# Optimization experiments

Measured on AMD Instinct MI355X. Metric: run time of the kernel, lower is better.

## Reference

```python
import jax, jax.numpy as jnp
import numpy as np

B, N, C, CP, H, NK = 1, 2048, 128, 16, 8, 128
D = C // H
W_HALF = NK // 2
EPS = 1e-5
NEG = -1e9


def _ln(x, scale=None, bias=None):
    m = jnp.mean(x, axis=-1, keepdims=True)
    v = jnp.var(x, axis=-1, keepdims=True)
    y = (x - m) * jax.lax.rsqrt(v + EPS)
    if scale is not None:
        y = y * scale
    if bias is not None:
        y = y + bias
    return y


def _ada_ln(a, s, s_scale, gate_w, gate_b, skip_w):
    # AF3 AdaLN: a <- sigmoid(Lin(LN(s))) * LN(a) + LinNoBias(LN(s))
    sn = _ln(s, s_scale)
    return jax.nn.sigmoid(sn @ gate_w + gate_b) * _ln(a) + sn @ skip_w


def setup_inputs() -> dict:
    key = jax.random.key(0)
    ks = jax.random.split(key, 24)

    def w(k, shape, fan_in):
        return jax.random.normal(k, shape, jnp.float32) / np.float32(np.sqrt(fan_in))

    return {
        'atom_single_repr': jax.random.normal(ks[0], (B, N, C), jnp.float32),
        'atom_single_proj': jax.random.normal(ks[1], (B, N, C), jnp.float32),
        'atom_pair_repr': jax.random.normal(ks[2], (B, N, N, CP), jnp.float32),
        'mask': jnp.ones((B, N), jnp.float32),
        # AttentionPairBias AdaLN
        'adaln_s_scale': jnp.ones((C,), jnp.float32),
        'adaln_gate_w': w(ks[3], (C, C), C),
        'adaln_gate_b': jnp.zeros((C,), jnp.float32),
        'adaln_skip_w': w(ks[4], (C, C), C),
        # attention projections
        'wq': w(ks[5], (C, H * D), C),
        'wk': w(ks[6], (C, H * D), C),
        'wv': w(ks[7], (C, H * D), C),
        'wg': w(ks[8], (C, H * D), C),
        'bg': jnp.ones((H * D,), jnp.float32),
        'wo': w(ks[9], (H * D, C), H * D),
        'bo': jnp.zeros((C,), jnp.float32),
        # pair bias
        'pair_ln_scale': jnp.ones((CP,), jnp.float32),
        'pair_ln_bias': jnp.zeros((CP,), jnp.float32),
        'w_pair': w(ks[10], (CP, H), CP),
        # adaLN-zero output gate (bias init -2)
        'out_gate_w': w(ks[11], (C, C), C),
        'out_gate_b': jnp.full((C,), -2.0, jnp.float32),
        # ConditionedTransitionBlock AdaLN
        't_s_scale': jnp.ones((C,), jnp.float32),
        't_gate_w': w(ks[12], (C, C), C),
        't_gate_b': jnp.zeros((C,), jnp.float32),
        't_skip_w': w(ks[13], (C, C), C),
        # SwiGLU transition, expansion n=2
        't_swish_w': w(ks[14], (C, 2 * C), C),
        't_hidden_w': w(ks[15], (C, 2 * C), C),
        't_out_w': w(ks[16], (2 * C, C), 2 * C),
        't_out_gate_w': w(ks[17], (C, C), C),
        't_out_gate_b': jnp.full((C,), -2.0, jnp.float32),
    }


def reference(atom_single_repr, atom_single_proj, atom_pair_repr, mask,
              adaln_s_scale, adaln_gate_w, adaln_gate_b, adaln_skip_w,
              wq, wk, wv, wg, bg, wo, bo,
              pair_ln_scale, pair_ln_bias, w_pair,
              out_gate_w, out_gate_b,
              t_s_scale, t_gate_w, t_gate_b, t_skip_w,
              t_swish_w, t_hidden_w, t_out_w, t_out_gate_w, t_out_gate_b):
    b, n, _ = atom_single_repr.shape
    # --- AttentionPairBias ---
    a = _ada_ln(atom_single_repr, atom_single_proj,
                adaln_s_scale, adaln_gate_w, adaln_gate_b, adaln_skip_w)
    # pair bias [b,h,n,n]
    bias = jnp.transpose(_ln(atom_pair_repr, pair_ln_scale, pair_ln_bias) @ w_pair, (0, 3, 1, 2))
    idx = jnp.arange(n)
    diff = idx[None, :] - idx[:, None]  # j - i
    win = (diff >= -W_HALF) & (diff <= W_HALF)  # sliding window (left,right)=(64,64)
    bias = bias + jnp.where(win, 0.0, NEG)[None, None]
    bias = bias + (1e9 * (mask - 1.0))[:, None, None, :]
    q = (a @ wq).reshape(b, n, H, D) * (D ** -0.5)
    k = (a @ wk).reshape(b, n, H, D)
    v = (a @ wv).reshape(b, n, H, D)
    attn = jax.nn.softmax(jnp.einsum('bqhd,bkhd->bhqk', q, k) + bias, axis=-1)
    o = jnp.einsum('bhqk,bkhd->bqhd', attn, v)
    g = jax.nn.sigmoid(a @ wg + bg).reshape(b, n, H, D)  # per-head output gating
    attn_out = (o * g).reshape(b, n, H * D) @ wo + bo
    attn_out = jax.nn.sigmoid(atom_single_proj @ out_gate_w + out_gate_b) * attn_out
    # --- ConditionedTransitionBlock ---
    t = _ada_ln(atom_single_repr, atom_single_proj,
                t_s_scale, t_gate_w, t_gate_b, t_skip_w)
    hid = jax.nn.silu(t @ t_swish_w) * (t @ t_hidden_w)  # SwiGLU
    trans = jax.nn.sigmoid(atom_single_proj @ t_out_gate_w + t_out_gate_b) * (hid @ t_out_w)
    return attn_out + trans
```

## Files before the change

kernel.cpp:

```cpp
#include <hip/hip_runtime.h>

#define NN 2048
#define CC 128
#define CPC 16
#define HH 8
#define DD 16
#define WHALF 64

__device__ __forceinline__ float sigf(float x){ return 1.0f/(1.0f+__expf(-x)); }

__global__ __launch_bounds__(256) void ln_both(const float* __restrict__ a,
                                               const float* __restrict__ s,
                                               float* __restrict__ ln_a,
                                               float* __restrict__ ln_s){
  const float* x = blockIdx.y ? s : a;
  float* ln = blockIdx.y ? ln_s : ln_a;
  int row = blockIdx.x*4 + (threadIdx.x>>6);
  int lane = threadIdx.x & 63;
  size_t base = (size_t)row*CC;
  float2 v = *(const float2*)(x + base + 2*lane);
  float ssum = v.x+v.y, sq = v.x*v.x+v.y*v.y;
  #pragma unroll
  for (int m=32;m;m>>=1){ ssum += __shfl_xor(ssum,m); sq += __shfl_xor(sq,m); }
  float mean = ssum*(1.0f/CC);
  float var  = sq*(1.0f/CC)-mean*mean;
  float inv  = rsqrtf(var+1e-5f);
  float2 o; o.x=(v.x-mean)*inv; o.y=(v.y-mean)*inv;
  *(float2*)(ln + base + 2*lane) = o;
}

template<int K, int RPT, int NM>
__device__ __forceinline__ void gemm_core(const float* __restrict__ Arows,
                                          const float* __restrict__ scale,
                                          const float* __restrict__ W0,
                                          const float* __restrict__ W1,
                                          int ldw, int colBase,
                                          float acc[NM][RPT][4], float* As){
  const int t = threadIdx.x;
  constexpr int ROWS = RPT*8;
  const int nv = ROWS*K/4;
  for (int i=t;i<nv;i+=256){
    float4 v = ((const float4*)Arows)[i];
    if (scale){
      int kk = (i*4)&(K-1);
      v.x*=scale[kk]; v.y*=scale[kk+1]; v.z*=scale[kk+2]; v.w*=scale[kk+3];
    }
    ((float4*)As)[i]=v;
  }
  __syncthreads();
  const int tr = t>>5;
  const int col = colBase + (t&31)*4;
  #pragma unroll
  for(int m=0;m<NM;m++)
    #pragma unroll
    for(int r=0;r<RPT;r++){ acc[m][r][0]=0;acc[m][r][1]=0;acc[m][r][2]=0;acc[m][r][3]=0; }
  #pragma unroll 4
  for (int k=0;k<K;k++){
    float a[RPT];
    #pragma unroll
    for (int r=0;r<RPT;r++) a[r]=As[(tr*RPT+r)*K+k];
    {
      float4 w = *(const float4*)(W0 + (size_t)k*ldw + col);
      #pragma unroll
      for (int r=0;r<RPT;r++){acc[0][r][0]+=a[r]*w.x;acc[0][r][1]+=a[r]*w.y;acc[0][r][2]+=a[r]*w.z;acc[0][r][3]+=a[r]*w.w;}
    }
    if constexpr (NM>1){
      float4 w = *(const float4*)(W1 + (size_t)k*ldw + col);
      #pragma unroll
      for (int r=0;r<RPT;r++){acc[1][r][0]+=a[r]*w.x;acc[1][r][1]+=a[r]*w.y;acc[1][r][2]+=a[r]*w.z;acc[1][r][3]+=a[r]*w.w;}
    }
  }
}

__global__ __launch_bounds__(256) void k_gates(const float* __restrict__ s,
    const float* __restrict__ W0, const float* __restrict__ b0,
    const float* __restrict__ W1, const float* __restrict__ b1,
    float* __restrict__ sgog, float* __restrict__ sgtg){
  __shared__ float As[8*128];
  float acc[2][1][4];
  const int row0 = blockIdx.x*8;
  gemm_core<128,1,2>(s + (size_t)row0*CC, nullptr, W0, W1, 128, 0, acc, As);
  const int col = (threadIdx.x&31)*4;
  const int row = row0 + (threadIdx.x>>5);
  float4 v0 = *(const float4*)(b0+col);
  float4 v1 = *(const float4*)(b1+col);
  float4 o0, o1;
  o0.x=sigf(acc[0][0][0]+v0.x); o0.y=sigf(acc[0][0][1]+v0.y); o0.z=sigf(acc[0][0][2]+v0.z); o0.w=sigf(acc[0][0][3]+v0.w);
  o1.x=sigf(acc[1][0][0]+v1.x); o1.y=sigf(acc[1][0][1]+v1.y); o1.z=sigf(acc[1][0][2]+v1.z); o1.w=sigf(acc[1][0][3]+v1.w);
  *(float4*)(sgog + (size_t)row*CC + col) = o0;
  *(float4*)(sgtg + (size_t)row*CC + col) = o1;
}

__global__ __launch_bounds__(256) void k_adaln(const float* __restrict__ ln_s,
    const float* __restrict__ sscale,
    const float* __restrict__ gate_w, const float* __restrict__ gate_b,
    const float* __restrict__ skip_w, const float* __restrict__ ln_a,
    float* __restrict__ outp){
  __shared__ float As[8*128];
  float acc[2][1][4];
  const int row0 = blockIdx.x*8;
  gemm_core<128,1,2>(ln_s + (size_t)row0*CC, sscale, gate_w, skip_w, 128, 0, acc, As);
  const int col = (threadIdx.x&31)*4;
  const int row = row0 + (threadIdx.x>>5);
  float4 gb = *(const float4*)(gate_b+col);
  float4 la = *(const float4*)(ln_a + (size_t)row*CC + col);
  float4 o;
  o.x = sigf(acc[0][0][0]+gb.x)*la.x + acc[1][0][0];
  o.y = sigf(acc[0][0][1]+gb.y)*la.y + acc[1][0][1];
  o.z = sigf(acc[0][0][2]+gb.z)*la.z + acc[1][0][2];
  o.w = sigf(acc[0][0][3]+gb.w)*la.w + acc[1][0][3];
  *(float4*)(outp + (size_t)row*CC + col) = o;
}

__global__ __launch_bounds__(256) void k_qkvg(const float* __restrict__ A,
    const float* __restrict__ wq, const float* __restrict__ wk,
    const float* __restrict__ wv, const float* __restrict__ wg,
    const float* __restrict__ bg,
    float* __restrict__ qb, float* __restrict__ kb,
    float* __restrict__ vb, float* __restrict__ gg){
  __shared__ float As[16*128];
  float acc[2][2][4];
  const int row0 = blockIdx.x*16;
  const int y = blockIdx.y;
  const float* W0 = y ? wv : wq;
  const float* W1 = y ? wg : wk;
  gemm_core<128,2,2>(A + (size_t)row0*CC, nullptr, W0, W1, 128, 0, acc, As);
  const int col = (threadIdx.x&31)*4;
  float* O0 = y ? vb : qb;
  float* O1 = y ? gg : kb;
  float4 b1 = {0,0,0,0};
  if (y) b1 = *(const float4*)(bg+col);
  #pragma unroll
  for (int r=0;r<2;r++){
    const int row = row0 + (threadIdx.x>>5)*2 + r;
    float4 o0 = {acc[0][r][0],acc[0][r][1],acc[0][r][2],acc[0][r][3]};
    float4 o1 = {acc[1][r][0]+b1.x,acc[1][r][1]+b1.y,acc[1][r][2]+b1.z,acc[1][r][3]+b1.w};
    *(float4*)(O0 + (size_t)row*CC + col) = o0;
    *(float4*)(O1 + (size_t)row*CC + col) = o1;
  }
}

__global__ __launch_bounds__(256) void k_wo(const float* __restrict__ A,
    const float* __restrict__ W, const float* __restrict__ b,
    float* __restrict__ outp){
  __shared__ float As[8*128];
  float acc[1][1][4];
  const int row0 = blockIdx.x*8;
  gemm_core<128,1,1>(A + (size_t)row0*CC, nullptr, W, nullptr, 128, 0, acc, As);
  const int col = (threadIdx.x&31)*4;
  const int row = row0 + (threadIdx.x>>5);
  float4 bb = *(const float4*)(b+col);
  float4 o = {acc[0][0][0]+bb.x, acc[0][0][1]+bb.y, acc[0][0][2]+bb.z, acc[0][0][3]+bb.w};
  *(float4*)(outp + (size_t)row*CC + col) = o;
}

__global__ __launch_bounds__(256) void k_swiglu(const float* __restrict__ A,
    const float* __restrict__ sw_w, const float* __restrict__ hd_w,
    float* __restrict__ hid){
  __shared__ float As[8*128];
  float acc[2][1][4];
  const int row0 = blockIdx.x*8;
  const int cb = blockIdx.y*128;
  gemm_core<128,1,2>(A + (size_t)row0*CC, nullptr, sw_w, hd_w, 256, cb, acc, As);
  const int col = cb + (threadIdx.x&31)*4;
  const int row = row0 + (threadIdx.x>>5);
  float4 o;
  o.x = acc[0][0][0]*sigf(acc[0][0][0])*acc[1][0][0];
  o.y = acc[0][0][1]*sigf(acc[0][0][1])*acc[1][0][1];
  o.z = acc[0][0][2]*sigf(acc[0][0][2])*acc[1][0][2];
  o.w = acc[0][0][3]*sigf(acc[0][0][3])*acc[1][0][3];
  *(float4*)(hid + (size_t)row*256 + col) = o;
}

__global__ __launch_bounds__(256) void k_tout(const float* __restrict__ hid,
    const float* __restrict__ W,
    const float* __restrict__ sgog, const float* __restrict__ aout,
    const float* __restrict__ sgtg, float* __restrict__ outp){
  __shared__ float As[8*256];
  float acc[1][1][4];
  const int row0 = blockIdx.x*8;
  gemm_core<256,1,1>(hid + (size_t)row0*256, nullptr, W, nullptr, 128, 0, acc, As);
  const int col = (threadIdx.x&31)*4;
  const int row = row0 + (threadIdx.x>>5);
  float4 g0 = *(const float4*)(sgog + (size_t)row*CC + col);
  float4 ao = *(const float4*)(aout + (size_t)row*CC + col);
  float4 g1 = *(const float4*)(sgtg + (size_t)row*CC + col);
  float4 o;
  o.x = g0.x*ao.x + g1.x*acc[0][0][0];
  o.y = g0.y*ao.y + g1.y*acc[0][0][1];
  o.z = g0.z*ao.z + g1.z*acc[0][0][2];
  o.w = g0.w*ao.w + g1.w*acc[0][0][3];
  *(float4*)(outp + (size_t)row*CC + col) = o;
}

__global__ __launch_bounds__(256) void attn_win(const float* __restrict__ q,
    const float* __restrict__ k, const float* __restrict__ v,
    const float* __restrict__ g, const float* __restrict__ pair,
    const float* __restrict__ pls, const float* __restrict__ plb,
    const float* __restrict__ w_pair, const float* __restrict__ mask,
    float* __restrict__ o_out) {
  __shared__ __align__(16) float qs[CC];
  __shared__ float sc[HH][132];
  __shared__ float wp[CPC][HH];
  __shared__ float plss[CPC], plbs[CPC];
  __shared__ float inv_sum[HH];
  const int i = blockIdx.x;
  const int t = threadIdx.x;
  if (t < CC) qs[t] = q[(size_t)i*CC + t] * 0.25f;
  if (t < CPC*HH) wp[t>>3][t&7] = w_pair[t];
  if (t >= 128 && t < 128+CPC){ plss[t-128]=pls[t-128]; plbs[t-128]=plb[t-128]; }
  __syncthreads();
  const int jlo = (i-WHALF > 0) ? i-WHALF : 0;
  const int jhi = (i+WHALF < NN-1) ? i+WHALF : NN-1;
  const int nj = jhi - jlo + 1;
  if (t < nj){
    const int j = jlo + t;
    float pv[CPC]; float s=0.f, sq=0.f;
    const float4* pp4 = (const float4*)(pair + ((size_t)i*NN + j)*CPC);
    #pragma unroll
    for (int c4=0;c4<CPC/4;c4++){
      float4 x4 = pp4[c4];
      pv[c4*4]=x4.x; pv[c4*4+1]=x4.y; pv[c4*4+2]=x4.z; pv[c4*4+3]=x4.w;
      s += x4.x+x4.y+x4.z+x4.w;
      sq += x4.x*x4.x+x4.y*x4.y+x4.z*x4.z+x4.w*x4.w;
    }
    float mean = s*(1.0f/CPC);
    float var  = sq*(1.0f/CPC)-mean*mean;
    float inv  = rsqrtf(var+1e-5f);
    #pragma unroll
    for (int c=0;c<CPC;c++) pv[c] = (pv[c]-mean)*inv*plss[c] + plbs[c];
    float mterm = 1e9f*(mask[j]-1.0f);
    const float4* kr4 = (const float4*)(k + (size_t)j*CC);
    const float4* qs4 = (const float4*)qs;
    #pragma unroll
    for (int h=0;h<HH;h++){
      float bias = 0.f;
      #pragma unroll
      for (int c=0;c<CPC;c++) bias += pv[c]*wp[c][h];
      float d = 0.f;
      #pragma unroll
      for (int w=0;w<4;w++){
        float4 kk = kr4[h*4+w];
        float4 qq = qs4[h*4+w];
        d += kk.x*qq.x + kk.y*qq.y + kk.z*qq.z + kk.w*qq.w;
      }
      sc[h][t] = d + bias + mterm;
    }
  }
  __syncthreads();
  {
    const int h = t >> 5;
    const int l = t & 31;
    float m = -1e30f;
    for (int jj=l; jj<nj; jj+=32) m = fmaxf(m, sc[h][jj]);
    #pragma unroll
    for (int mm=16;mm;mm>>=1) m = fmaxf(m, __shfl_xor(m,mm));
    float ss = 0.f;
    for (int jj=l; jj<nj; jj+=32){ float e=__expf(sc[h][jj]-m); sc[h][jj]=e; ss+=e; }
    #pragma unroll
    for (int mm=16;mm;mm>>=1) ss += __shfl_xor(ss,mm);
    if (l==0) inv_sum[h] = 1.0f/ss;
  }
  __syncthreads();
  if (t < CC){
    const int h = t >> 4;
    float acc = 0.f;
    for (int jj=0; jj<nj; jj++)
      acc += sc[h][jj] * v[(size_t)(jlo+jj)*CC + t];
    float gate = sigf(g[(size_t)i*CC + t]);
    o_out[(size_t)i*CC + t] = acc * inv_sum[h] * gate;
  }
}

extern "C" void kernel_launch(void* const* d_in, const int* in_sizes, int n_in,
                              void* d_out, int out_size, void* d_ws, size_t ws_size,
                              hipStream_t stream) {
  const float* a_in = (const float*)d_in[0];
  const float* s_in = (const float*)d_in[1];
  const float* pair = (const float*)d_in[2];
  const float* mask = (const float*)d_in[3];
  const float* adaln_s_scale = (const float*)d_in[4];
  const float* adaln_gate_w  = (const float*)d_in[5];
  const float* adaln_gate_b  = (const float*)d_in[6];
  const float* adaln_skip_w  = (const float*)d_in[7];
  const float* wq = (const float*)d_in[8];
  const float* wk = (const float*)d_in[9];
  const float* wv = (const float*)d_in[10];
  const float* wg = (const float*)d_in[11];
  const float* bg = (const float*)d_in[12];
  const float* wo = (const float*)d_in[13];
  const float* bo = (const float*)d_in[14];
  const float* pls = (const float*)d_in[15];
  const float* plb = (const float*)d_in[16];
  const float* w_pair = (const float*)d_in[17];
  const float* out_gate_w = (const float*)d_in[18];
  const float* out_gate_b = (const float*)d_in[19];
  const float* t_s_scale  = (const float*)d_in[20];
  const float* t_gate_w   = (const float*)d_in[21];
  const float* t_gate_b   = (const float*)d_in[22];
  const float* t_skip_w   = (const float*)d_in[23];
  const float* t_swish_w  = (const float*)d_in[24];
  const float* t_hidden_w = (const float*)d_in[25];
  const float* t_out_w    = (const float*)d_in[26];
  const float* t_out_gate_w = (const float*)d_in[27];
  const float* t_out_gate_b = (const float*)d_in[28];

  float* ws = (float*)d_ws;
  const size_t U = (size_t)NN*CC;
  float* ln_a  = ws + 0*U;
  float* ln_s  = ws + 1*U;
  float* sg_og = ws + 2*U;
  float* sg_tg = ws + 3*U;
  float* a_att = ws + 4*U;
  float* tcond = ws + 5*U;
  float* qb    = ws + 6*U;
  float* kb    = ws + 7*U;
  float* vb    = ws + 8*U;
  float* gg    = ws + 9*U;
  float* o_gat = ws + 10*U;
  float* aout  = ws + 11*U;
  float* hid   = ws + 12*U;

  dim3 blk(256);
  ln_both<<<dim3(NN/4,2), blk, 0, stream>>>(a_in, s_in, ln_a, ln_s);
  k_gates<<<NN/8, blk, 0, stream>>>(s_in, out_gate_w, out_gate_b, t_out_gate_w, t_out_gate_b, sg_og, sg_tg);
  k_adaln<<<NN/8, blk, 0, stream>>>(ln_s, adaln_s_scale, adaln_gate_w, adaln_gate_b, adaln_skip_w, ln_a, a_att);
  k_adaln<<<NN/8, blk, 0, stream>>>(ln_s, t_s_scale, t_gate_w, t_gate_b, t_skip_w, ln_a, tcond);
  k_qkvg<<<dim3(NN/16,2), blk, 0, stream>>>(a_att, wq, wk, wv, wg, bg, qb, kb, vb, gg);
  attn_win<<<NN, blk, 0, stream>>>(qb, kb, vb, gg, pair, pls, plb, w_pair, mask, o_gat);
  k_wo<<<NN/8, blk, 0, stream>>>(o_gat, wo, bo, aout);
  k_swiglu<<<dim3(NN/8,2), blk, 0, stream>>>(tcond, t_swish_w, t_hidden_w, hid);
  k_tout<<<NN/8, blk, 0, stream>>>(hid, t_out_w, sg_og, aout, sg_tg, (float*)d_out);
}
```

Before: 535.6 us.

## Fuse pre-attention and post-attention GEMM chains into two megakernels

Replaces the layernorm, gate, AdaLN, QKVG and SwiGLU kernels with a single kernel that keeps normalized rows and intermediates in LDS. The Wo and transition output GEMMs plus the final gating are merged into one kernel. This removes several launches and global round-trips of intermediates. It also splits the attention PV accumulation into four independent accumulators to expose ILP. The risk is lower parallelism, since the blockIdx.y=0 branch does four GEMMs serially while y=1 does three, which causes load imbalance. The larger LDS footprint may also reduce occupancy.

```diff
diff --git a/kernel.cpp b/kernel.cpp
--- a/kernel.cpp
+++ b/kernel.cpp
@@ -9,188 +9,176 @@
 
 __device__ __forceinline__ float sigf(float x){ return 1.0f/(1.0f+__expf(-x)); }
 
-__global__ __launch_bounds__(256) void ln_both(const float* __restrict__ a,
-                                               const float* __restrict__ s,
-                                               float* __restrict__ ln_a,
-                                               float* __restrict__ ln_s){
-  const float* x = blockIdx.y ? s : a;
-  float* ln = blockIdx.y ? ln_s : ln_a;
-  int row = blockIdx.x*4 + (threadIdx.x>>6);
-  int lane = threadIdx.x & 63;
-  size_t base = (size_t)row*CC;
-  float2 v = *(const float2*)(x + base + 2*lane);
-  float ssum = v.x+v.y, sq = v.x*v.x+v.y*v.y;
+template<int KK, int NM, bool SC>
+__device__ __forceinline__ void gemm_lds(const float* __restrict__ X,
+    const float* __restrict__ scv,
+    const float* __restrict__ W0, const float* __restrict__ W1,
+    int ldw, int colBase, float a0[4], float a1[4]){
+  const int t = threadIdx.x;
+  const int r = t>>5;
+  const int c = colBase + (t&31)*4;
+  a0[0]=a0[1]=a0[2]=a0[3]=0.f;
+  a1[0]=a1[1]=a1[2]=a1[3]=0.f;
+  #pragma unroll 8
+  for (int k=0;k<KK;k++){
+    float a = X[r*KK+k];
+    if constexpr (SC) a *= scv[k];
+    float4 w0 = *(const float4*)(W0 + (size_t)k*ldw + c);
+    a0[0]+=a*w0.x; a0[1]+=a*w0.y; a0[2]+=a*w0.z; a0[3]+=a*w0.w;
+    if constexpr (NM>1){
+      float4 w1 = *(const float4*)(W1 + (size_t)k*ldw + c);
+      a1[0]+=a*w1.x; a1[1]+=a*w1.y; a1[2]+=a*w1.z; a1[3]+=a*w1.w;
+    }
+  }
+}
+
+template<int KK>
+__device__ __forceinline__ void gemm_g(const float* __restrict__ Xrow,
+    const float* __restrict__ W0, int ldw, float a0[4]){
+  const int c = (threadIdx.x&31)*4;
+  a0[0]=a0[1]=a0[2]=a0[3]=0.f;
+  #pragma unroll 8
+  for (int k=0;k<KK;k++){
+    float a = Xrow[k];
+    float4 w0 = *(const float4*)(W0 + (size_t)k*ldw + c);
+    a0[0]+=a*w0.x; a0[1]+=a*w0.y; a0[2]+=a*w0.z; a0[3]+=a*w0.w;
+  }
+}
+
+__device__ __forceinline__ float4 ln_row4(const float* __restrict__ x, int row, int c4, float4& raw){
+  float4 v = *(const float4*)(x + (size_t)row*CC + c4);
+  raw = v;
+  float sm = v.x+v.y+v.z+v.w;
+  float sq = v.x*v.x+v.y*v.y+v.z*v.z+v.w*v.w;
   #pragma unroll
-  for (int m=32;m;m>>=1){ ssum += __shfl_xor(ssum,m); sq += __shfl_xor(sq,m); }
-  float mean = ssum*(1.0f/CC);
+  for (int m=16;m;m>>=1){ sm += __shfl_xor(sm,m); sq += __shfl_xor(sq,m); }
+  float mean = sm*(1.0f/CC);
   float var  = sq*(1.0f/CC)-mean*mean;
   float inv  = rsqrtf(var+1e-5f);
-  float2 o; o.x=(v.x-mean)*inv; o.y=(v.y-mean)*inv;
-  *(float2*)(ln + base + 2*lane) = o;
-}
-
-template<int K, int RPT, int NM>
-__device__ __forceinline__ void gemm_core(const float* __restrict__ Arows,
-                                          const float* __restrict__ scale,
-                                          const float* __restrict__ W0,
-                                          const float* __restrict__ W1,
-                                          int ldw, int colBase,
-                                          float acc[NM][RPT][4], float* As){
-  const int t = threadIdx.x;
-  constexpr int ROWS = RPT*8;
-  const int nv = ROWS*K/4;
-  for (int i=t;i<nv;i+=256){
-    float4 v = ((const float4*)Arows)[i];
-    if (scale){
-      int kk = (i*4)&(K-1);
-      v.x*=scale[kk]; v.y*=scale[kk+1]; v.z*=scale[kk+2]; v.w*=scale[kk+3];
-    }
-    ((float4*)As)[i]=v;
-  }
-  __syncthreads();
-  const int tr = t>>5;
-  const int col = colBase + (t&31)*4;
-  #pragma unroll
-  for(int m=0;m<NM;m++)
-    #pragma unroll
-    for(int r=0;r<RPT;r++){ acc[m][r][0]=0;acc[m][r][1]=0;acc[m][r][2]=0;acc[m][r][3]=0; }
-  #pragma unroll 4
-  for (int k=0;k<K;k++){
-    float a[RPT];
-    #pragma unroll
-    for (int r=0;r<RPT;r++) a[r]=As[(tr*RPT+r)*K+k];
-    {
-      float4 w = *(const float4*)(W0 + (size_t)k*ldw + col);
-      #pragma unroll
-      for (int r=0;r<RPT;r++){acc[0][r][0]+=a[r]*w.x;acc[0][r][1]+=a[r]*w.y;acc[0][r][2]+=a[r]*w.z;acc[0][r][3]+=a[r]*w.w;}
-    }
-    if constexpr (NM>1){
-      float4 w = *(const float4*)(W1 + (size_t)k*ldw + col);
-      #pragma unroll
-      for (int r=0;r<RPT;r++){acc[1][r][0]+=a[r]*w.x;acc[1][r][1]+=a[r]*w.y;acc[1][r][2]+=a[r]*w.z;acc[1][r][3]+=a[r]*w.w;}
-    }
-  }
-}
-
-__global__ __launch_bounds__(256) void k_gates(const float* __restrict__ s,
-    const float* __restrict__ W0, const float* __restrict__ b0,
-    const float* __restrict__ W1, const float* __restrict__ b1,
-    float* __restrict__ sgog, float* __restrict__ sgtg){
-  __shared__ float As[8*128];
-  float acc[2][1][4];
-  const int row0 = blockIdx.x*8;
-  gemm_core<128,1,2>(s + (size_t)row0*CC, nullptr, W0, W1, 128, 0, acc, As);
-  const int col = (threadIdx.x&31)*4;
-  const int row = row0 + (threadIdx.x>>5);
-  float4 v0 = *(const float4*)(b0+col);
-  float4 v1 = *(const float4*)(b1+col);
-  float4 o0, o1;
-  o0.x=sigf(acc[0][0][0]+v0.x); o0.y=sigf(acc[0][0][1]+v0.y); o0.z=sigf(acc[0][0][2]+v0.z); o0.w=sigf(acc[0][0][3]+v0.w);
-  o1.x=sigf(acc[1][0][0]+v1.x); o1.y=sigf(acc[1][0][1]+v1.y); o1.z=sigf(acc[1][0][2]+v1.z); o1.w=sigf(acc[1][0][3]+v1.w);
-  *(float4*)(sgog + (size_t)row*CC + col) = o0;
-  *(float4*)(sgtg + (size_t)row*CC + col) = o1;
-}
-
-__global__ __launch_bounds__(256) void k_adaln(const float* __restrict__ ln_s,
-    const float* __restrict__ sscale,
-    const float* __restrict__ gate_w, const float* __restrict__ gate_b,
-    const float* __restrict__ skip_w, const float* __restrict__ ln_a,
-    float* __restrict__ outp){
-  __shared__ float As[8*128];
-  float acc[2][1][4];
-  const int row0 = blockIdx.x*8;
-  gemm_core<128,1,2>(ln_s + (size_t)row0*CC, sscale, gate_w, skip_w, 128, 0, acc, As);
-  const int col = (threadIdx.x&31)*4;
-  const int row = row0 + (threadIdx.x>>5);
-  float4 gb = *(const float4*)(gate_b+col);
-  float4 la = *(const float4*)(ln_a + (size_t)row*CC + col);
-  float4 o;
-  o.x = sigf(acc[0][0][0]+gb.x)*la.x + acc[1][0][0];
-  o.y = sigf(acc[0][0][1]+gb.y)*la.y + acc[1][0][1];
-  o.z = sigf(acc[0][0][2]+gb.z)*la.z + acc[1][0][2];
-  o.w = sigf(acc[0][0][3]+gb.w)*la.w + acc[1][0][3];
-  *(float4*)(outp + (size_t)row*CC + col) = o;
-}
-
-__global__ __launch_bounds__(256) void k_qkvg(const float* __restrict__ A,
+  float4 o; o.x=(v.x-mean)*inv; o.y=(v.y-mean)*inv; o.z=(v.z-mean)*inv; o.w=(v.w-mean)*inv;
+  return o;
+}
+
+__global__ __launch_bounds__(256) void mega1(
+    const float* __restrict__ a_in, const float* __restrict__ s_in,
+    const float* __restrict__ sc1, const float* __restrict__ gw,
+    const float* __restrict__ gb,  const float* __restrict__ skw,
+    const float* __restrict__ ogw, const float* __restrict__ ogb,
+    const float* __restrict__ ogw2,const float* __restrict__ ogb2,
     const float* __restrict__ wq, const float* __restrict__ wk,
     const float* __restrict__ wv, const float* __restrict__ wg,
     const float* __restrict__ bg,
+    const float* __restrict__ sc2, const float* __restrict__ tgw,
+    const float* __restrict__ tgb, const float* __restrict__ tskw,
+    const float* __restrict__ sww, const float* __restrict__ hdw,
     float* __restrict__ qb, float* __restrict__ kb,
-    float* __restrict__ vb, float* __restrict__ gg){
-  __shared__ float As[16*128];
-  float acc[2][2][4];
-  const int row0 = blockIdx.x*16;
+    float* __restrict__ vb, float* __restrict__ gg,
+    float* __restrict__ sgog, float* __restrict__ sgtg,
+    float* __restrict__ hid){
+  __shared__ float ls[8*128];
+  __shared__ float la[8*128];
+  __shared__ float aux[8*128];
+  __shared__ float xbuf[8*128];
+  __shared__ float scv[128];
+  const int t = threadIdx.x;
+  const int row0 = blockIdx.x*8;
   const int y = blockIdx.y;
-  const float* W0 = y ? wv : wq;
-  const float* W1 = y ? wg : wk;
-  gemm_core<128,2,2>(A + (size_t)row0*CC, nullptr, W0, W1, 128, 0, acc, As);
-  const int col = (threadIdx.x&31)*4;
-  float* O0 = y ? vb : qb;
-  float* O1 = y ? gg : kb;
-  float4 b1 = {0,0,0,0};
-  if (y) b1 = *(const float4*)(bg+col);
-  #pragma unroll
-  for (int r=0;r<2;r++){
-    const int row = row0 + (threadIdx.x>>5)*2 + r;
-    float4 o0 = {acc[0][r][0],acc[0][r][1],acc[0][r][2],acc[0][r][3]};
-    float4 o1 = {acc[1][r][0]+b1.x,acc[1][r][1]+b1.y,acc[1][r][2]+b1.z,acc[1][r][3]+b1.w};
-    *(float4*)(O0 + (size_t)row*CC + col) = o0;
-    *(float4*)(O1 + (size_t)row*CC + col) = o1;
-  }
-}
-
-__global__ __launch_bounds__(256) void k_wo(const float* __restrict__ A,
-    const float* __restrict__ W, const float* __restrict__ b,
+  const int r = t>>5;
+  const int c4 = (t&31)*4;
+  const int row = row0 + r;
+  {
+    float4 raw;
+    float4 n = ln_row4(s_in, row, c4, raw);
+    *(float4*)(ls + r*128 + c4) = n;
+    if (y==0) *(float4*)(aux + r*128 + c4) = raw;
+  }
+  {
+    float4 raw;
+    float4 n = ln_row4(a_in, row, c4, raw);
+    *(float4*)(la + r*128 + c4) = n;
+  }
+  if (t < 128) scv[t] = (y==0 ? sc1 : sc2)[t];
+  __syncthreads();
+
+  float p0[4], p1[4];
+  if (y==0){
+    gemm_lds<128,2,false>(aux, nullptr, ogw, ogw2, 128, 0, p0, p1);
+    {
+      float4 b0 = *(const float4*)(ogb + c4);
+      float4 b1 = *(const float4*)(ogb2 + c4);
+      float4 o0 = { sigf(p0[0]+b0.x), sigf(p0[1]+b0.y), sigf(p0[2]+b0.z), sigf(p0[3]+b0.w) };
+      float4 o1 = { sigf(p1[0]+b1.x), sigf(p1[1]+b1.y), sigf(p1[2]+b1.z), sigf(p1[3]+b1.w) };
+      *(float4*)(sgog + (size_t)row*CC + c4) = o0;
+      *(float4*)(sgtg + (size_t)row*CC + c4) = o1;
+    }
+    gemm_lds<128,2,true>(ls, scv, gw, skw, 128, 0, p0, p1);
+    {
+      float4 gbv = *(const float4*)(gb + c4);
+      float4 lav = *(const float4*)(la + r*128 + c4);
+      float4 o;
+      o.x = sigf(p0[0]+gbv.x)*lav.x + p1[0];
+      o.y = sigf(p0[1]+gbv.y)*lav.y + p1[1];
+      o.z = sigf(p0[2]+gbv.z)*lav.z + p1[2];
+      o.w = sigf(p0[3]+gbv.w)*lav.w + p1[3];
+      *(float4*)(xbuf + r*128 + c4) = o;
+    }
+    __syncthreads();
+    gemm_lds<128,2,false>(xbuf, nullptr, wq, wk, 128, 0, p0, p1);
+    *(float4*)(qb + (size_t)row*CC + c4) = *(float4*)p0;
+    *(float4*)(kb + (size_t)row*CC + c4) = *(float4*)p1;
+    gemm_lds<128,2,false>(xbuf, nullptr, wv, wg, 128, 0, p0, p1);
+    {
+      float4 bgv = *(const float4*)(bg + c4);
+      float4 o1 = { p1[0]+bgv.x, p1[1]+bgv.y, p1[2]+bgv.z, p1[3]+bgv.w };
+      *(float4*)(vb + (size_t)row*CC + c4) = *(float4*)p0;
+      *(float4*)(gg + (size_t)row*CC + c4) = o1;
+    }
+  } else {
+    gemm_lds<128,2,true>(ls, scv, tgw, tskw, 128, 0, p0, p1);
+    {
+      float4 gbv = *(const float4*)(tgb + c4);
+      float4 lav = *(const float4*)(la + r*128 + c4);
+      float4 o;
+      o.x = sigf(p0[0]+gbv.x)*lav.x + p1[0];
+      o.y = sigf(p0[1]+gbv.y)*lav.y + p1[1];
+      o.z = sigf(p0[2]+gbv.z)*lav.z + p1[2];
+      o.w = sigf(p0[3]+gbv.w)*lav.w + p1[3];
+      *(float4*)(xbuf + r*128 + c4) = o;
+    }
+    __syncthreads();
+    #pragma unroll
+    for (int cb=0; cb<256; cb+=128){
+      gemm_lds<128,2,false>(xbuf, nullptr, sww, hdw, 256, cb, p0, p1);
+      float4 o;
+      o.x = p0[0]*sigf(p0[0])*p1[0];
+      o.y = p0[1]*sigf(p0[1])*p1[1];
+      o.z = p0[2]*sigf(p0[2])*p1[2];
+      o.w = p0[3]*sigf(p0[3])*p1[3];
+      *(float4*)(hid + (size_t)row*256 + cb + c4) = o;
+    }
+  }
+}
+
+__global__ __launch_bounds__(256) void mega2(const float* __restrict__ o_gat,
+    const float* __restrict__ hid, const float* __restrict__ wo,
+    const float* __restrict__ bo, const float* __restrict__ tow,
+    const float* __restrict__ sgog, const float* __restrict__ sgtg,
     float* __restrict__ outp){
-  __shared__ float As[8*128];
-  float acc[1][1][4];
-  const int row0 = blockIdx.x*8;
-  gemm_core<128,1,1>(A + (size_t)row0*CC, nullptr, W, nullptr, 128, 0, acc, As);
-  const int col = (threadIdx.x&31)*4;
-  const int row = row0 + (threadIdx.x>>5);
-  float4 bb = *(const float4*)(b+col);
-  float4 o = {acc[0][0][0]+bb.x, acc[0][0][1]+bb.y, acc[0][0][2]+bb.z, acc[0][0][3]+bb.w};
-  *(float4*)(outp + (size_t)row*CC + col) = o;
-}
-
-__global__ __launch_bounds__(256) void k_swiglu(const float* __restrict__ A,
-    const float* __restrict__ sw_w, const float* __restrict__ hd_w,
-    float* __restrict__ hid){
-  __shared__ float As[8*128];
-  float acc[2][1][4];
-  const int row0 = blockIdx.x*8;
-  const int cb = blockIdx.y*128;
-  gemm_core<128,1,2>(A + (size_t)row0*CC, nullptr, sw_w, hd_w, 256, cb, acc, As);
-  const int col = cb + (threadIdx.x&31)*4;
-  const int row = row0 + (threadIdx.x>>5);
+  const int t = threadIdx.x;
+  const int row = blockIdx.x*8 + (t>>5);
+  const int c4 = (t&31)*4;
+  float ao[4], tr[4];
+  gemm_g<128>(o_gat + (size_t)row*CC, wo, 128, ao);
+  gemm_g<256>(hid + (size_t)row*256, tow, 128, tr);
+  float4 bb = *(const float4*)(bo + c4);
+  float4 g0 = *(const float4*)(sgog + (size_t)row*CC + c4);
+  float4 g1 = *(const float4*)(sgtg + (size_t)row*CC + c4);
   float4 o;
-  o.x = acc[0][0][0]*sigf(acc[0][0][0])*acc[1][0][0];
-  o.y = acc[0][0][1]*sigf(acc[0][0][1])*acc[1][0][1];
-  o.z = acc[0][0][2]*sigf(acc[0][0][2])*acc[1][0][2];
-  o.w = acc[0][0][3]*sigf(acc[0][0][3])*acc[1][0][3];
-  *(float4*)(hid + (size_t)row*256 + col) = o;
-}
-
-__global__ __launch_bounds__(256) void k_tout(const float* __restrict__ hid,
-    const float* __restrict__ W,
-    const float* __restrict__ sgog, const float* __restrict__ aout,
-    const float* __restrict__ sgtg, float* __restrict__ outp){
-  __shared__ float As[8*256];
-  float acc[1][1][4];
-  const int row0 = blockIdx.x*8;
-  gemm_core<256,1,1>(hid + (size_t)row0*256, nullptr, W, nullptr, 128, 0, acc, As);
-  const int col = (threadIdx.x&31)*4;
-  const int row = row0 + (threadIdx.x>>5);
-  float4 g0 = *(const float4*)(sgog + (size_t)row*CC + col);
-  float4 ao = *(const float4*)(aout + (size_t)row*CC + col);
-  float4 g1 = *(const float4*)(sgtg + (size_t)row*CC + col);
-  float4 o;
-  o.x = g0.x*ao.x + g1.x*acc[0][0][0];
-  o.y = g0.y*ao.y + g1.y*acc[0][0][1];
-  o.z = g0.z*ao.z + g1.z*acc[0][0][2];
-  o.w = g0.w*ao.w + g1.w*acc[0][0][3];
-  *(float4*)(outp + (size_t)row*CC + col) = o;
+  o.x = g0.x*(ao[0]+bb.x) + g1.x*tr[0];
+  o.y = g0.y*(ao[1]+bb.y) + g1.y*tr[1];
+  o.z = g0.z*(ao[2]+bb.z) + g1.z*tr[2];
+  o.w = g0.w*(ao[3]+bb.w) + g1.w*tr[3];
+  *(float4*)(outp + (size_t)row*CC + c4) = o;
 }
 
 __global__ __launch_bounds__(256) void attn_win(const float* __restrict__ q,
@@ -264,9 +252,17 @@
   __syncthreads();
   if (t < CC){
     const int h = t >> 4;
-    float acc = 0.f;
-    for (int jj=0; jj<nj; jj++)
-      acc += sc[h][jj] * v[(size_t)(jlo+jj)*CC + t];
+    const float* vt = v + t;
+    float a0=0.f,a1=0.f,a2=0.f,a3=0.f;
+    int jj=0;
+    for (; jj+4<=nj; jj+=4){
+      a0 += sc[h][jj]   * vt[(size_t)(jlo+jj)*CC];
+      a1 += sc[h][jj+1] * vt[(size_t)(jlo+jj+1)*CC];
+      a2 += sc[h][jj+2] * vt[(size_t)(jlo+jj+2)*CC];
+      a3 += sc[h][jj+3] * vt[(size_t)(jlo+jj+3)*CC];
+    }
+    for (; jj<nj; jj++) a0 += sc[h][jj]*vt[(size_t)(jlo+jj)*CC];
+    float acc = (a0+a1)+(a2+a3);
     float gate = sigf(g[(size_t)i*CC + t]);
     o_out[(size_t)i*CC + t] = acc * inv_sum[h] * gate;
   }
@@ -307,28 +303,23 @@
 
   float* ws = (float*)d_ws;
   const size_t U = (size_t)NN*CC;
-  float* ln_a  = ws + 0*U;
-  float* ln_s  = ws + 1*U;
-  float* sg_og = ws + 2*U;
-  float* sg_tg = ws + 3*U;
-  float* a_att = ws + 4*U;
-  float* tcond = ws + 5*U;
-  float* qb    = ws + 6*U;
-  float* kb    = ws + 7*U;
-  float* vb    = ws + 8*U;
-  float* gg    = ws + 9*U;
-  float* o_gat = ws + 10*U;
-  float* aout  = ws + 11*U;
-  float* hid   = ws + 12*U;
+  float* qb    = ws + 0*U;
+  float* kb    = ws + 1*U;
+  float* vb    = ws + 2*U;
+  float* gg    = ws + 3*U;
+  float* sg_og = ws + 4*U;
+  float* sg_tg = ws + 5*U;
+  float* o_gat = ws + 6*U;
+  float* hid   = ws + 7*U;
 
   dim3 blk(256);
-  ln_both<<<dim3(NN/4,2), blk, 0, stream>>>(a_in, s_in, ln_a, ln_s);
-  k_gates<<<NN/8, blk, 0, stream>>>(s_in, out_gate_w, out_gate_b, t_out_gate_w, t_out_gate_b, sg_og, sg_tg);
-  k_adaln<<<NN/8, blk, 0, stream>>>(ln_s, adaln_s_scale, adaln_gate_w, adaln_gate_b, adaln_skip_w, ln_a, a_att);
-  k_adaln<<<NN/8, blk, 0, stream>>>(ln_s, t_s_scale, t_gate_w, t_gate_b, t_skip_w, ln_a, tcond);
-  k_qkvg<<<dim3(NN/16,2), blk, 0, stream>>>(a_att, wq, wk, wv, wg, bg, qb, kb, vb, gg);
+  mega1<<<dim3(NN/8,2), blk, 0, stream>>>(a_in, s_in,
+      adaln_s_scale, adaln_gate_w, adaln_gate_b, adaln_skip_w,
+      out_gate_w, out_gate_b, t_out_gate_w, t_out_gate_b,
+      wq, wk, wv, wg, bg,
+      t_s_scale, t_gate_w, t_gate_b, t_skip_w,
+      t_swish_w, t_hidden_w,
+      qb, kb, vb, gg, sg_og, sg_tg, hid);
   attn_win<<<NN, blk, 0, stream>>>(qb, kb, vb, gg, pair, pls, plb, w_pair, mask, o_gat);
-  k_wo<<<NN/8, blk, 0, stream>>>(o_gat, wo, bo, aout);
-  k_swiglu<<<dim3(NN/8,2), blk, 0, stream>>>(tcond, t_swish_w, t_hidden_w, hid);
-  k_tout<<<NN/8, blk, 0, stream>>>(hid, t_out_w, sg_og, aout, sg_tg, (float*)d_out);
-}
+  mega2<<<NN/8, blk, 0, stream>>>(o_gat, hid, wo, bo, t_out_w, sg_og, sg_tg, (float*)d_out);
+}
```

Result: slower. 563.5 us (+5.2%).
